# Kernel tuning notes

Hardware: AMD Instinct MI355X
Metric: run time of the kernel (lower is better)

The kernel has to match this reference:

```python
import jax, jax.numpy as jnp
import numpy as np

B, T, DM, H, DH = 4, 2048, 1024, 16, 64
DI = H * DH
CLIP = 1.0
LN_EPS = 1e-5


def setup_inputs() -> dict:
    key = jax.random.key(0)
    ks = jax.random.split(key, 9)

    def xav(k, shape):  # xavier_uniform, fan_in=shape[1], fan_out=shape[0]
        lim = float(np.sqrt(6.0 / (shape[0] + shape[1])))
        return jax.random.uniform(k, shape, jnp.float32, -lim, lim)

    def kai(k, shape):  # default nn.Linear weight init
        lim = float(1.0 / np.sqrt(shape[1]))
        return jax.random.uniform(k, shape, jnp.float32, -lim, lim)

    return {
        "x": jax.random.normal(ks[0], (B, T, DM), jnp.float32),
        "Wq": xav(ks[1], (DI, DM)),
        "Wk": xav(ks[2], (DI, DM)),
        "Wv": xav(ks[3], (DI, DM)),
        "Wa": kai(ks[4], (DI, DM)), "ba": jnp.full((DI,), 3.0, jnp.float32),
        "Wb": kai(ks[5], (H, DM)), "bb": jnp.zeros((H,), jnp.float32),
        "Wg": kai(ks[6], (H, DM)), "bg": jnp.zeros((H,), jnp.float32),
        "WaR": kai(ks[7], (DI, DM)), "baR": jnp.full((DI,), 3.0, jnp.float32),
        "Wo": xav(ks[8], (DM, DI)),
        "ln_w": jnp.ones((DM,), jnp.float32),
        "ln_b": jnp.zeros((DM,), jnp.float32),
    }


def reference(x, Wq, Wk, Wv, Wa, ba, Wb, bb, Wg, bg, WaR, baR, Wo, ln_w, ln_b):
    Bs, Ts, _ = x.shape
    residual = x
    # LayerNorm
    mu = jnp.mean(x, -1, keepdims=True)
    var = jnp.mean((x - mu) ** 2, -1, keepdims=True)
    xn = (x - mu) / jnp.sqrt(var + LN_EPS) * ln_w + ln_b

    q = (xn @ Wq.T).reshape(Bs, Ts, H, DH)
    k = (xn @ Wk.T).reshape(Bs, Ts, H, DH)
    v = (xn @ Wv.T).reshape(Bs, Ts, H, DH)
    alpha = jax.nn.sigmoid(xn @ Wa.T + ba).reshape(Bs, Ts, H, DH)
    aR = jax.nn.sigmoid(xn @ WaR.T + baR).reshape(Bs, Ts, H, DH)
    beta = jax.nn.sigmoid(xn @ Wb.T + bb)   # (B,T,H)
    gamma = jax.nn.sigmoid(xn @ Wg.T + bg)  # (B,T,H)

    tm = lambda a: jnp.moveaxis(a, 1, 0)  # time-major for scan
    xs = (tm(q), tm(k), tm(v), tm(alpha), tm(aR), tm(beta), tm(gamma))
    S0 = jnp.zeros((Bs, H, DH, DH), x.dtype)

    def step(carry, inp):
        S, R = carry
        q_t, k_t, v_t, a_t, aR_t, b_t, g_t = inp  # (B,H,d) / (B,H)
        kn = k_t / jnp.maximum(jnp.linalg.norm(k_t, axis=-1, keepdims=True), 1e-12)
        # residual target from previous state: r = clip(v - S^T k)
        pred = jnp.einsum('bhji,bhj->bhi', S, kn)
        r = jnp.clip(v_t - pred, -CLIP, CLIP)
        # primary state: S = diag(alpha) S; S += beta k (v - k^T S)
        S = a_t[..., None] * S
        kp = jnp.einsum('bhd,bhde->bhe', kn, S)
        S = S + b_t[..., None, None] * kn[..., None] * (v_t - kp)[..., None, :]
        o = jnp.einsum('bhji,bhj->bhi', S, q_t)
        # residual state
        R = aR_t[..., None] * R
        kpR = jnp.einsum('bhd,bhde->bhe', kn, R)
        R = R + g_t[..., None, None] * kn[..., None] * (r - kpR)[..., None, :]
        o = o + jnp.einsum('bhji,bhj->bhi', R, q_t)
        return (S, R), o

    _, os = jax.lax.scan(step, (S0, S0), xs)  # os: (T,B,H,d)
    out = jnp.moveaxis(os, 0, 1).reshape(Bs, Ts, DI) @ Wo.T
    return out + residual  # dropout is identity at inference
```

## Files before the change

kernel.cpp:

```cpp
#include <hip/hip_runtime.h>
#include <hip/hip_fp16.h>

#define B_SZ 4
#define T_SEQ 2048
#define NH 16
#define HD 64
#define DMODEL 1024
#define MTOT (B_SZ * T_SEQ)

typedef __bf16 bf16x8 __attribute__((ext_vector_type(8)));
typedef float f32x4 __attribute__((ext_vector_type(4)));
typedef float f32x2 __attribute__((ext_vector_type(2)));
typedef _Float16 f16x4 __attribute__((ext_vector_type(4)));

__device__ __forceinline__ unsigned short f2bf(float f) {
    union { float f; unsigned int i; } c; c.f = f;
    unsigned int u = c.i;
    u += 0x7fffu + ((u >> 16) & 1u);
    return (unsigned short)(u >> 16);
}
__device__ __forceinline__ float sigm(float x) { return 1.f / (1.f + __expf(-x)); }

__device__ __forceinline__ void dma16(const void* g, void* l) {
    __builtin_amdgcn_global_load_lds(
        (const __attribute__((address_space(1))) void*)g,
        (__attribute__((address_space(3))) void*)l, 16, 0, 0);
}

template <int CTRL>
__device__ __forceinline__ float dppadd(float x) {
    int v = __builtin_amdgcn_update_dpp(0, __builtin_bit_cast(int, x), CTRL, 0xf, 0xf, false);
    return x + __builtin_bit_cast(float, v);
}
__device__ __forceinline__ float rowsum16(float x) {
    x = dppadd<0x128>(x);
    x = dppadd<0x124>(x);
    x = dppadd<0x122>(x);
    x = dppadd<0x121>(x);
    return x;
}

__device__ __forceinline__ void rowsum3(float& a, float& b, float& c) {
    asm volatile(
        "s_nop 1\n\t"
        "v_add_f32_dpp %0, %0, %0 row_ror:8 row_mask:0xf bank_mask:0xf\n\t"
        "v_add_f32_dpp %1, %1, %1 row_ror:8 row_mask:0xf bank_mask:0xf\n\t"
        "v_add_f32_dpp %2, %2, %2 row_ror:8 row_mask:0xf bank_mask:0xf\n\t"
        "v_add_f32_dpp %0, %0, %0 row_ror:4 row_mask:0xf bank_mask:0xf\n\t"
        "v_add_f32_dpp %1, %1, %1 row_ror:4 row_mask:0xf bank_mask:0xf\n\t"
        "v_add_f32_dpp %2, %2, %2 row_ror:4 row_mask:0xf bank_mask:0xf\n\t"
        "v_add_f32_dpp %0, %0, %0 row_ror:2 row_mask:0xf bank_mask:0xf\n\t"
        "v_add_f32_dpp %1, %1, %1 row_ror:2 row_mask:0xf bank_mask:0xf\n\t"
        "v_add_f32_dpp %2, %2, %2 row_ror:2 row_mask:0xf bank_mask:0xf\n\t"
        "v_add_f32_dpp %0, %0, %0 row_ror:1 row_mask:0xf bank_mask:0xf\n\t"
        "v_add_f32_dpp %1, %1, %1 row_ror:1 row_mask:0xf bank_mask:0xf\n\t"
        "v_add_f32_dpp %2, %2, %2 row_ror:1 row_mask:0xf bank_mask:0xf"
        : "+v"(a), "+v"(b), "+v"(c));
}

__global__ __launch_bounds__(256, 1) void k_ln(const float* __restrict__ x,
                                               const float* __restrict__ lnw,
                                               const float* __restrict__ lnb,
                                               unsigned short* __restrict__ xn) {
    const int m = blockIdx.x;
    const int t = threadIdx.x;
    float4 xv = ((const float4*)(x + (size_t)m * DMODEL))[t];
    float s = xv.x + xv.y + xv.z + xv.w;
    float s2 = xv.x * xv.x + xv.y * xv.y + xv.z * xv.z + xv.w * xv.w;
#pragma unroll
    for (int off = 32; off >= 1; off >>= 1) {
        s += __shfl_xor(s, off);
        s2 += __shfl_xor(s2, off);
    }
    __shared__ float red[8];
    const int wid = t >> 6;
    if ((t & 63) == 0) { red[wid] = s; red[4 + wid] = s2; }
    __syncthreads();
    if (t == 0) {
        float su = red[0] + red[1] + red[2] + red[3];
        float sq = red[4] + red[5] + red[6] + red[7];
        float mu = su * (1.f / DMODEL);
        float var = sq * (1.f / DMODEL) - mu * mu;
        red[0] = mu;
        red[1] = rsqrtf(var + 1e-5f);
    }
    __syncthreads();
    float mu = red[0], rstd = red[1];
    float4 w4 = ((const float4*)lnw)[t];
    float4 b4 = ((const float4*)lnb)[t];
    ushort4 o;
    o.x = f2bf((xv.x - mu) * rstd * w4.x + b4.x);
    o.y = f2bf((xv.y - mu) * rstd * w4.y + b4.y);
    o.z = f2bf((xv.z - mu) * rstd * w4.z + b4.z);
    o.w = f2bf((xv.w - mu) * rstd * w4.w + b4.w);
    ((ushort4*)(xn + (size_t)m * DMODEL))[t] = o;
}

struct WPtrs { const float* p0; const float* p1; const float* p2; const float* p3; const float* p4; };

__global__ __launch_bounds__(256, 1) void k_wconv(WPtrs w, unsigned short* __restrict__ dst) {
    const int plane = blockIdx.y;
    const float* src = plane == 0 ? w.p0 : plane == 1 ? w.p1 : plane == 2 ? w.p2
                                                             : plane == 3 ? w.p3 : w.p4;
    const size_t i = ((size_t)blockIdx.x * 256 + threadIdx.x) * 8;
    float4 f0 = *(const float4*)(src + i);
    float4 f1 = *(const float4*)(src + i + 4);
    uint4 o;
    o.x = (unsigned)f2bf(f0.x) | ((unsigned)f2bf(f0.y) << 16);
    o.y = (unsigned)f2bf(f0.z) | ((unsigned)f2bf(f0.w) << 16);
    o.z = (unsigned)f2bf(f1.x) | ((unsigned)f2bf(f1.y) << 16);
    o.w = (unsigned)f2bf(f1.z) | ((unsigned)f2bf(f1.w) << 16);
    *(uint4*)(dst + (size_t)plane * 1048576 + i) = o;
}

__global__ __launch_bounds__(256, 1) void k_cvt1(const float* __restrict__ src,
                                                 unsigned short* __restrict__ dst) {
    const size_t i = ((size_t)blockIdx.x * 256 + threadIdx.x) * 8;
    float4 f0 = *(const float4*)(src + i);
    float4 f1 = *(const float4*)(src + i + 4);
    uint4 o;
    o.x = (unsigned)f2bf(f0.x) | ((unsigned)f2bf(f0.y) << 16);
    o.y = (unsigned)f2bf(f0.z) | ((unsigned)f2bf(f0.w) << 16);
    o.z = (unsigned)f2bf(f1.x) | ((unsigned)f2bf(f1.y) << 16);
    o.w = (unsigned)f2bf(f1.z) | ((unsigned)f2bf(f1.w) << 16);
    *(uint4*)(dst + i) = o;
}

template <int KDIM>
__device__ __forceinline__ void gemm128(const unsigned short* __restrict__ A,
                                        const unsigned short* __restrict__ Bw,
                                        int m0, int n0, f32x4 acc[4][4]) {
    __shared__ __align__(16) unsigned short sA[128 * 32];
    __shared__ __align__(16) unsigned short sB[128 * 32];

    const int t = threadIdx.x;
    const int lane = t & 63;
    const int wv = t >> 6;
    const int wm = wv >> 1, wn = wv & 1;
    const int ml = lane & 15, kq = lane >> 4;

#pragma unroll
    for (int i = 0; i < 4; i++)
#pragma unroll
        for (int j = 0; j < 4; j++) {
            f32x4 z; z[0] = 0.f; z[1] = 0.f; z[2] = 0.f; z[3] = 0.f;
            acc[i][j] = z;
        }

    const unsigned short* pA = A + (size_t)m0 * KDIM;
    const unsigned short* pB = Bw + (size_t)n0 * KDIM;
    const unsigned short* gA0 = pA + (size_t)(t >> 2) * KDIM + (t & 3) * 8;
    const unsigned short* gA1 = gA0 + (size_t)64 * KDIM;
    const unsigned short* gB0 = pB + (size_t)(t >> 2) * KDIM + (t & 3) * 8;
    const unsigned short* gB1 = gB0 + (size_t)64 * KDIM;
    unsigned short* lA0 = sA + wv * 512;
    unsigned short* lA1 = lA0 + 2048;
    unsigned short* lB0 = sB + wv * 512;
    unsigned short* lB1 = lB0 + 2048;

    for (int kb = 0; kb < KDIM / 32; kb++) {
        const int ko = kb * 32;
        dma16(gA0 + ko, lA0);
        dma16(gA1 + ko, lA1);
        dma16(gB0 + ko, lB0);
        dma16(gB1 + ko, lB1);
        __syncthreads();
        bf16x8 af[4], bfr[4];
#pragma unroll
        for (int mt = 0; mt < 4; mt++)
            af[mt] = *(const bf16x8*)&sA[(wm * 64 + mt * 16 + ml) * 32 + kq * 8];
#pragma unroll
        for (int nt = 0; nt < 4; nt++)
            bfr[nt] = *(const bf16x8*)&sB[(wn * 64 + nt * 16 + ml) * 32 + kq * 8];
#pragma unroll
        for (int mt = 0; mt < 4; mt++)
#pragma unroll
            for (int nt = 0; nt < 4; nt++)
                acc[mt][nt] = __builtin_amdgcn_mfma_f32_16x16x32_bf16(af[mt], bfr[nt], acc[mt][nt], 0, 0, 0);
        __syncthreads();
    }
}

template <typename OT>
__global__ __launch_bounds__(256, 1) void k_proj(const unsigned short* __restrict__ xn,
                                                 const unsigned short* __restrict__ wbf,
                                                 const float* __restrict__ ba,
                                                 const float* __restrict__ baR,
                                                 OT* __restrict__ qo, OT* __restrict__ ko,
                                                 OT* __restrict__ vo, OT* __restrict__ ao,
                                                 OT* __restrict__ aRo) {
    const int m0 = blockIdx.x * 128;
    const int yt = blockIdx.y;
    const int widx = yt >> 3;
    const int n0 = (yt & 7) * 128;
    const unsigned short* W = wbf + (size_t)widx * 1048576;
    f32x4 acc[4][4];
    gemm128<1024>(xn, W, m0, n0, acc);

    OT* outp = widx == 0 ? qo : widx == 1 ? ko : widx == 2 ? vo : widx == 3 ? ao : aRo;
    const float* bias = (widx == 3) ? ba : (widx == 4) ? baR : (const float*)0;
    const int lane = threadIdx.x & 63;
    const int wv = threadIdx.x >> 6;
    const int wm = wv >> 1, wn = wv & 1;
    const int ml = lane & 15, kq = lane >> 4;
#pragma unroll
    for (int mt = 0; mt < 4; mt++)
#pragma unroll
        for (int nt = 0; nt < 4; nt++) {
            const int rowg = m0 + wm * 64 + mt * 16 + kq * 4;
            const int colg = n0 + wn * 64 + nt * 16 + ml;
            float bval = bias ? bias[colg] : 0.f;
#pragma unroll
            for (int r = 0; r < 4; r++) {
                float v = acc[mt][nt][r];
                if (widx >= 3) v = sigm(v + bval);
                outp[(size_t)(rowg + r) * DMODEL + colg] = (OT)v;
            }
        }
}

__global__ __launch_bounds__(256, 1) void k_bg(const unsigned short* __restrict__ xn,
                                               const float* __restrict__ Wb,
                                               const float* __restrict__ bb,
                                               const float* __restrict__ Wg,
                                               const float* __restrict__ bgp,
                                               f32x2* __restrict__ bgpk) {
    const int m = blockIdx.x;
    const int t = threadIdx.x;
    const int h = t >> 4, seg = t & 15;
    const ushort4* xr = (const ushort4*)(xn + (size_t)m * DMODEL + seg * 64);
    const float4* wbr = (const float4*)(Wb + (size_t)h * DMODEL + seg * 64);
    const float4* wgr = (const float4*)(Wg + (size_t)h * DMODEL + seg * 64);
    float db = 0.f, dg = 0.f;
#pragma unroll
    for (int u = 0; u < 16; u++) {
        ushort4 a = xr[u];
        float4 w1 = wbr[u], w2 = wgr[u];
        union { unsigned int i; float f; } c0, c1, c2, c3;
        c0.i = ((unsigned int)a.x) << 16; c1.i = ((unsigned int)a.y) << 16;
        c2.i = ((unsigned int)a.z) << 16; c3.i = ((unsigned int)a.w) << 16;
        db += c0.f * w1.x + c1.f * w1.y + c2.f * w1.z + c3.f * w1.w;
        dg += c0.f * w2.x + c1.f * w2.y + c2.f * w2.z + c3.f * w2.w;
    }
#pragma unroll
    for (int off = 1; off < 16; off <<= 1) {
        db += __shfl_xor(db, off);
        dg += __shfl_xor(dg, off);
    }
    if (seg == 0) {
        f32x2 o;
        o[0] = sigm(db + bb[h]);
        o[1] = sigm(dg + bgp[h]);
        bgpk[(size_t)m * NH + h] = o;
    }
}

__global__ __launch_bounds__(256, 1) void k_prep16(__half* __restrict__ kb) {
    const int row = blockIdx.x * 16 + (threadIdx.x >> 4);
    const int tr = threadIdx.x & 15;
    const int bh = row >> 11, t = row & 2047;
    const size_t idx = ((size_t)((bh >> 4) * T_SEQ + t)) * DMODEL + (bh & 15) * 64 + tr * 4;
    f16x4 k4 = *(const f16x4*)((const __half*)kb + idx);
    float k0 = (float)k4[0], k1 = (float)k4[1], k2 = (float)k4[2], k3 = (float)k4[3];
    float ss = k0 * k0 + k1 * k1 + k2 * k2 + k3 * k3;
    ss = rowsum16(ss);
    float inv = 1.f / fmaxf(sqrtf(ss), 1e-12f);
    f16x4 o;
    o[0] = (_Float16)(k0 * inv); o[1] = (_Float16)(k1 * inv);
    o[2] = (_Float16)(k2 * inv); o[3] = (_Float16)(k3 * inv);
    *(f16x4*)(kb + idx) = o;
}

__global__ __launch_bounds__(256, 1) void k_prep32(float* __restrict__ kb) {
    const int row = blockIdx.x * 16 + (threadIdx.x >> 4);
    const int tr = threadIdx.x & 15;
    const int bh = row >> 11, t = row & 2047;
    const size_t idx = ((size_t)((bh >> 4) * T_SEQ + t)) * DMODEL + (bh & 15) * 64 + tr * 4;
    f32x4 k4 = *(const f32x4*)(kb + idx);
    float ss = k4[0] * k4[0] + k4[1] * k4[1] + k4[2] * k4[2] + k4[3] * k4[3];
    ss = rowsum16(ss);
    float inv = 1.f / fmaxf(sqrtf(ss), 1e-12f);
    f32x4 o;
    o[0] = k4[0] * inv; o[1] = k4[1] * inv; o[2] = k4[2] * inv; o[3] = k4[3] * inv;
    *(f32x4*)(kb + idx) = o;
}

__global__ __launch_bounds__(256, 1) void k_scan32(const float* __restrict__ qb,
                                                   const float* __restrict__ knb,
                                                   const float* __restrict__ vb,
                                                   const float* __restrict__ ab,
                                                   const float* __restrict__ aRb,
                                                   const f32x2* __restrict__ bgpk,
                                                   unsigned short* __restrict__ ob) {
    const int blk = blockIdx.x;
    const int bh = blk & 63, cg = blk >> 6;
    const int b = bh >> 4, h = bh & 15;
    const int t = threadIdx.x;
    const int col = t >> 4, tr = t & 15;
    const int ii = cg * 16 + col;
    const int j0 = tr * 4;

    const size_t blkoff = (size_t)b * T_SEQ * DMODEL + h * 64;
    const float* pq = qb + blkoff;
    const float* pk = knb + blkoff;
    const float* pa = ab + blkoff;
    const float* pr = aRb + blkoff;
    const float* pvb = vb + blkoff;
    const f32x2* pbg = bgpk + (size_t)b * T_SEQ * NH + h;
    unsigned short* obp = ob + blkoff + ii;

    f32x2 S01 = {0.f, 0.f}, S23 = {0.f, 0.f}, R01 = {0.f, 0.f}, R23 = {0.f, 0.f};

    f32x4 rk[6], rq[6], ra[6], rr[6];
    float rv[6];
    f32x2 rbg[6];

#pragma unroll
    for (int p = 0; p < 6; p++) {
        const size_t vo = (size_t)p * DMODEL;
        rk[p] = *(const f32x4*)(pk + vo + j0);
        rq[p] = *(const f32x4*)(pq + vo + j0);
        ra[p] = *(const f32x4*)(pa + vo + j0);
        rr[p] = *(const f32x4*)(pr + vo + j0);
        rv[p] = pvb[vo + ii];
        rbg[p] = pbg[(size_t)p * NH];
    }

    float oA, oB, oC;

#define SCAN_BODY32(P, ODEST)                                                       \
    {                                                                               \
        const f32x2 kn01 = {rk[P][0], rk[P][1]}, kn23 = {rk[P][2], rk[P][3]};       \
        const f32x2 a01 = {ra[P][0], ra[P][1]}, a23 = {ra[P][2], ra[P][3]};         \
        const f32x2 x01 = {rr[P][0], rr[P][1]}, x23 = {rr[P][2], rr[P][3]};         \
        const f32x2 q01 = {rq[P][0], rq[P][1]}, q23 = {rq[P][2], rq[P][3]};         \
        const float vc = rv[P];                                                     \
        const float beta = rbg[P][0], gamma = rbg[P][1];                            \
        const f32x2 Sd01 = a01 * S01, Sd23 = a23 * S23;                             \
        const f32x2 Rd01 = x01 * R01, Rd23 = x23 * R23;                             \
        const f32x2 pv2 = S01 * kn01 + S23 * kn23;                                  \
        const f32x2 kp2 = Sd01 * kn01 + Sd23 * kn23;                                \
        const f32x2 kR2 = Rd01 * kn01 + Rd23 * kn23;                                \
        float pred = pv2[0] + pv2[1];                                               \
        float kp = kp2[0] + kp2[1];                                                 \
        float kpR = kR2[0] + kR2[1];                                                \
        rowsum3(pred, kp, kpR);                                                     \
        const float rres = fminf(fmaxf(vc - pred, -1.f), 1.f);                      \
        const float cS = beta * (vc - kp);                                          \
        const float cR = gamma * (rres - kpR);                                      \
        const f32x2 cS2 = {cS, cS}, cR2 = {cR, cR};                                 \
        S01 = cS2 * kn01 + Sd01; S23 = cS2 * kn23 + Sd23;                           \
        R01 = cR2 * kn01 + Rd01; R23 = cR2 * kn23 + Rd23;                           \
        const f32x2 ov = (S01 + R01) * q01 + (S23 + R23) * q23;                     \
        ODEST = ov[0] + ov[1];                                                      \
              \
        {                                                                           \
            const int sp = (st + (P) + 6) & (T_SEQ - 1);                            \
            const size_t vo = (size_t)sp * DMODEL;                                  \
            rk[P] = *(const f32x4*)(pk + vo + j0);                                  \
            rq[P] = *(const f32x4*)(pq + vo + j0);                                  \
            ra[P] = *(const f32x4*)(pa + vo + j0);                                  \
            rr[P] = *(const f32x4*)(pr + vo + j0);                                  \
            rv[P] = pvb[vo + ii];                                                   \
            rbg[P] = pbg[(size_t)sp * NH];                                          \
        }                                                                           \
    }

#define FLUSH3(SBASE)                                                               \
    {                                                                               \
        rowsum3(oA, oB, oC);                                                        \
        if (tr == 0) {                                                              \
            if ((SBASE) < T_SEQ)     obp[(size_t)(SBASE) * DMODEL] = f2bf(oA);      \
            if ((SBASE) + 1 < T_SEQ) obp[(size_t)((SBASE) + 1) * DMODEL] = f2bf(oB);\
            if ((SBASE) + 2 < T_SEQ) obp[(size_t)((SBASE) + 2) * DMODEL] = f2bf(oC);\
        }                                                                           \
    }

    for (int st = 0; st < T_SEQ; st += 6) {
        SCAN_BODY32(0, oA)
        SCAN_BODY32(1, oB)
        SCAN_BODY32(2, oC)
        FLUSH3(st)
        SCAN_BODY32(3, oA)
        SCAN_BODY32(4, oB)
        SCAN_BODY32(5, oC)
        FLUSH3(st + 3)
    }
#undef SCAN_BODY32
#undef FLUSH3
}

__global__ __launch_bounds__(256, 1) void k_scan16(const __half* __restrict__ qb,
                                                   const __half* __restrict__ knb,
                                                   const __half* __restrict__ vb,
                                                   const __half* __restrict__ ab,
                                                   const __half* __restrict__ aRb,
                                                   const f32x2* __restrict__ bgpk,
                                                   unsigned short* __restrict__ ob) {
    const int blk = blockIdx.x;
    const int bh = blk & 63, cg = blk >> 6;
    const int b = bh >> 4, h = bh & 15;
    const int t = threadIdx.x;
    const int col = t >> 4, tr = t & 15;
    const int ii = cg * 16 + col;
    const int j0 = tr * 4;

    const size_t vecbase = ((size_t)b * T_SEQ) * DMODEL + h * 64 + j0;
    const size_t vbase = ((size_t)b * T_SEQ) * DMODEL + h * 64 + ii;
    const size_t bgbase = ((size_t)b * T_SEQ) * NH + h;

    const __half* pk = knb + vecbase;
    const __half* pq = qb + vecbase;
    const __half* pa = ab + vecbase;
    const __half* pr = aRb + vecbase;

    float S0 = 0, S1 = 0, S2 = 0, S3 = 0, R0 = 0, R1 = 0, R2 = 0, R3 = 0;

    f16x4 rk[6], rq[6], ra[6], rr[6];
    __half rv[6];
    f32x2 rbg[6];
    f32x4 fkn[6], fq[6], fa[6], fr[6];
    float fv[6];

#pragma unroll
    for (int p = 0; p < 6; p++) {
        const size_t voff = (size_t)p * DMODEL;
        rk[p] = *(const f16x4*)(pk + voff);
        rq[p] = *(const f16x4*)(pq + voff);
        ra[p] = *(const f16x4*)(pa + voff);
        rr[p] = *(const f16x4*)(pr + voff);
        rv[p] = vb[vbase + voff];
        rbg[p] = bgpk[bgbase + (size_t)p * NH];
    }
    fkn[0][0] = (float)rk[0][0]; fkn[0][1] = (float)rk[0][1]; fkn[0][2] = (float)rk[0][2]; fkn[0][3] = (float)rk[0][3];
    fq[0][0] = (float)rq[0][0]; fq[0][1] = (float)rq[0][1]; fq[0][2] = (float)rq[0][2]; fq[0][3] = (float)rq[0][3];
    fa[0][0] = (float)ra[0][0]; fa[0][1] = (float)ra[0][1]; fa[0][2] = (float)ra[0][2]; fa[0][3] = (float)ra[0][3];
    fr[0][0] = (float)rr[0][0]; fr[0][1] = (float)rr[0][1]; fr[0][2] = (float)rr[0][2]; fr[0][3] = (float)rr[0][3];
    fv[0] = (float)rv[0];

#define SCAN_BODY(P, PN)                                                              \
    {                                                                                 \
        const int s = st + (P);                                                       \
        const float beta = rbg[P][0], gamma = rbg[P][1];                              \
        {                                                                             \
            const size_t voff = (size_t)((s + 6) & (T_SEQ - 1)) * DMODEL;             \
            rk[P] = *(const f16x4*)(pk + voff);                                       \
            rq[P] = *(const f16x4*)(pq + voff);                                       \
            ra[P] = *(const f16x4*)(pa + voff);                                       \
            rr[P] = *(const f16x4*)(pr + voff);                                       \
            rv[P] = vb[vbase + voff];                                                 \
        }                                                                             \
        fkn[PN][0] = (float)rk[PN][0]; fkn[PN][1] = (float)rk[PN][1];                 \
        fkn[PN][2] = (float)rk[PN][2]; fkn[PN][3] = (float)rk[PN][3];                 \
        fq[PN][0] = (float)rq[PN][0]; fq[PN][1] = (float)rq[PN][1];                   \
        fq[PN][2] = (float)rq[PN][2]; fq[PN][3] = (float)rq[PN][3];                   \
        fa[PN][0] = (float)ra[PN][0]; fa[PN][1] = (float)ra[PN][1];                   \
        fa[PN][2] = (float)ra[PN][2]; fa[PN][3] = (float)ra[PN][3];                   \
        fr[PN][0] = (float)rr[PN][0]; fr[PN][1] = (float)rr[PN][1];                   \
        fr[PN][2] = (float)rr[PN][2]; fr[PN][3] = (float)rr[PN][3];                   \
        fv[PN] = (float)rv[PN];                                                       \
        {                                                                             \
            const float kn0 = fkn[P][0], kn1 = fkn[P][1], kn2 = fkn[P][2], kn3 = fkn[P][3]; \
            const float a0 = fa[P][0], a1 = fa[P][1], a2 = fa[P][2], a3 = fa[P][3];   \
            const float x0 = fr[P][0], x1 = fr[P][1], x2 = fr[P][2], x3 = fr[P][3];   \
            const float vc = fv[P];                                                   \
            float pred = S0 * kn0 + S1 * kn1 + S2 * kn2 + S3 * kn3;                   \
            float Sd0 = a0 * S0, Sd1 = a1 * S1, Sd2 = a2 * S2, Sd3 = a3 * S3;         \
            float Rd0 = x0 * R0, Rd1 = x1 * R1, Rd2 = x2 * R2, Rd3 = x3 * R3;         \
            float kp = Sd0 * kn0 + Sd1 * kn1 + Sd2 * kn2 + Sd3 * kn3;                 \
            float kpR = Rd0 * kn0 + Rd1 * kn1 + Rd2 * kn2 + Rd3 * kn3;                \
            pred = rowsum16(pred);                                                    \
            kp = rowsum16(kp);                                                        \
            kpR = rowsum16(kpR);                                                      \
            const float rres = fminf(fmaxf(vc - pred, -1.f), 1.f);                    \
            const float cS = beta * (vc - kp);                                        \
            const float cR = gamma * (rres - kpR);                                    \
            S0 = fmaf(cS, kn0, Sd0); S1 = fmaf(cS, kn1, Sd1);                         \
            S2 = fmaf(cS, kn2, Sd2); S3 = fmaf(cS, kn3, Sd3);                         \
            R0 = fmaf(cR, kn0, Rd0); R1 = fmaf(cR, kn1, Rd1);                         \
            R2 = fmaf(cR, kn2, Rd2); R3 = fmaf(cR, kn3, Rd3);                         \
            float o = (S0 + R0) * fq[P][0] + (S1 + R1) * fq[P][1] +                   \
                      (S2 + R2) * fq[P][2] + (S3 + R3) * fq[P][3];                    \
            o = rowsum16(o);                                                          \
            if (tr == 0 && s < T_SEQ)                                                 \
                ob[vbase + (size_t)s * DMODEL] = f2bf(o);                             \
        }                                                                             \
        rbg[P] = bgpk[bgbase + (size_t)((s + 6) & (T_SEQ - 1)) * NH];                 \
    }

    for (int st = 0; st < T_SEQ; st += 6) {
        SCAN_BODY(0, 1)
        SCAN_BODY(1, 2)
        SCAN_BODY(2, 3)
        SCAN_BODY(3, 4)
        SCAN_BODY(4, 5)
        SCAN_BODY(5, 0)
    }
#undef SCAN_BODY
}

__global__ __launch_bounds__(256, 1) void k_out(const unsigned short* __restrict__ ob,
                                                const unsigned short* __restrict__ wobf,
                                                const float* __restrict__ x,
                                                float* __restrict__ out) {
    const int m0 = blockIdx.x * 128;
    const int n0 = blockIdx.y * 128;
    f32x4 acc[4][4];
    gemm128<1024>(ob, wobf, m0, n0, acc);
    const int lane = threadIdx.x & 63;
    const int wv = threadIdx.x >> 6;
    const int wm = wv >> 1, wn = wv & 1;
    const int ml = lane & 15, kq = lane >> 4;
#pragma unroll
    for (int mt = 0; mt < 4; mt++)
#pragma unroll
        for (int nt = 0; nt < 4; nt++) {
            const int rowg = m0 + wm * 64 + mt * 16 + kq * 4;
            const int colg = n0 + wn * 64 + nt * 16 + ml;
#pragma unroll
            for (int r = 0; r < 4; r++) {
                size_t idx = (size_t)(rowg + r) * DMODEL + colg;
                out[idx] = acc[mt][nt][r] + x[idx];
            }
        }
}

extern "C" void kernel_launch(void* const* d_in, const int* in_sizes, int n_in,
                              void* d_out, int out_size, void* d_ws, size_t ws_size,
                              hipStream_t stream) {
    const float* x = (const float*)d_in[0];
    const float* Wq = (const float*)d_in[1];
    const float* Wk = (const float*)d_in[2];
    const float* Wv = (const float*)d_in[3];
    const float* Wa = (const float*)d_in[4];
    const float* ba = (const float*)d_in[5];
    const float* Wb = (const float*)d_in[6];
    const float* bb = (const float*)d_in[7];
    const float* Wg = (const float*)d_in[8];
    const float* bg = (const float*)d_in[9];
    const float* WaR = (const float*)d_in[10];
    const float* baR = (const float*)d_in[11];
    const float* Wo = (const float*)d_in[12];
    const float* lnw = (const float*)d_in[13];
    const float* lnb = (const float*)d_in[14];

    const size_t SZH = 16777216ULL;
    const size_t SZF = 33554432ULL;
    const size_t need32 = 5 * SZF + SZH + 2097152ULL;
    const size_t need16 = 6 * SZH + 2097152ULL;

    char* ws = (char*)d_ws;
    unsigned short* wbf = (unsigned short*)d_out;
    WPtrs wp{Wq, Wk, Wv, Wa, WaR};

    if (ws_size >= need32) {
        float* qb = (float*)(ws + 0 * SZF);
        float* kb = (float*)(ws + 1 * SZF);
        float* vb = (float*)(ws + 2 * SZF);
        float* ab = (float*)(ws + 3 * SZF);
        float* aRb = (float*)(ws + 4 * SZF);
        unsigned short* xn = (unsigned short*)(ws + 5 * SZF);
        f32x2* bgpk = (f32x2*)(ws + 5 * SZF + SZH);
        unsigned short* wobf = (unsigned short*)qb;

        k_wconv<<<dim3(512, 5), dim3(256), 0, stream>>>(wp, wbf);
        k_ln<<<dim3(MTOT), dim3(256), 0, stream>>>(x, lnw, lnb, xn);
        k_proj<float><<<dim3(64, 40), dim3(256), 0, stream>>>(xn, wbf, ba, baR, qb, kb, vb, ab, aRb);
        k_bg<<<dim3(MTOT), dim3(256), 0, stream>>>(xn, Wb, bb, Wg, bg, bgpk);
        k_prep32<<<dim3(MTOT * NH / 16), dim3(256), 0, stream>>>(kb);
        k_scan32<<<dim3(256), dim3(256), 0, stream>>>(qb, kb, vb, ab, aRb, bgpk, xn);
        k_cvt1<<<dim3(512), dim3(256), 0, stream>>>(Wo, wobf);
        k_out<<<dim3(64, 8), dim3(256), 0, stream>>>(xn, wobf, x, (float*)d_out);
    } else if (ws_size >= need16) {
        __half* qb = (__half*)(ws + 0 * SZH);
        __half* kb = (__half*)(ws + 1 * SZH);
        __half* vb = (__half*)(ws + 2 * SZH);
        __half* ab = (__half*)(ws + 3 * SZH);
        __half* aRb = (__half*)(ws + 4 * SZH);
        unsigned short* xn = (unsigned short*)(ws + 5 * SZH);
        f32x2* bgpk = (f32x2*)(ws + 6 * SZH);
        unsigned short* wobf = (unsigned short*)qb;

        k_wconv<<<dim3(512, 5), dim3(256), 0, stream>>>(wp, wbf);
        k_ln<<<dim3(MTOT), dim3(256), 0, stream>>>(x, lnw, lnb, xn);
        k_proj<_Float16><<<dim3(64, 40), dim3(256), 0, stream>>>(
            xn, wbf, ba, baR, (_Float16*)qb, (_Float16*)kb, (_Float16*)vb, (_Float16*)ab, (_Float16*)aRb);
        k_bg<<<dim3(MTOT), dim3(256), 0, stream>>>(xn, Wb, bb, Wg, bg, bgpk);
        k_prep16<<<dim3(MTOT * NH / 16), dim3(256), 0, stream>>>(kb);
        k_scan16<<<dim3(256), dim3(256), 0, stream>>>(qb, kb, vb, ab, aRb, bgpk, xn);
        k_cvt1<<<dim3(512), dim3(256), 0, stream>>>(Wo, wobf);
        k_out<<<dim3(64, 8), dim3(256), 0, stream>>>(xn, wobf, x, (float*)d_out);
    }
}
```

Before: 831.3 us.

## Double-buffer LDS tiles in gemm128 to overlap global loads with MFMA

Result: no change. 826.1 us (-0.6%).

```diff
diff --git a/kernel.cpp b/kernel.cpp
--- a/kernel.cpp
+++ b/kernel.cpp
@@ -130,8 +130,8 @@
 __device__ __forceinline__ void gemm128(const unsigned short* __restrict__ A,
                                         const unsigned short* __restrict__ Bw,
                                         int m0, int n0, f32x4 acc[4][4]) {
-    __shared__ __align__(16) unsigned short sA[128 * 32];
-    __shared__ __align__(16) unsigned short sB[128 * 32];
+    __shared__ __align__(16) unsigned short sA[2 * 128 * 32];
+    __shared__ __align__(16) unsigned short sB[2 * 128 * 32];
 
     const int t = threadIdx.x;
     const int lane = t & 63;
@@ -158,26 +158,43 @@
     unsigned short* lB0 = sB + wv * 512;
     unsigned short* lB1 = lB0 + 2048;
 
-    for (int kb = 0; kb < KDIM / 32; kb++) {
-        const int ko = kb * 32;
-        dma16(gA0 + ko, lA0);
-        dma16(gA1 + ko, lA1);
-        dma16(gB0 + ko, lB0);
-        dma16(gB1 + ko, lB1);
-        __syncthreads();
+    constexpr int NK = KDIM / 32;
+
+    dma16(gA0, lA0);
+    dma16(gA1, lA1);
+    dma16(gB0, lB0);
+    dma16(gB1, lB1);
+    asm volatile("s_waitcnt vmcnt(0)" ::: "memory");
+    __builtin_amdgcn_s_barrier();
+
+    int cur = 0;
+    for (int kb = 0; kb < NK; kb++) {
+        const int nxt = cur ^ 1;
+        if (kb + 1 < NK) {
+            const int ko = (kb + 1) * 32;
+            const int bo = nxt * 4096;
+            dma16(gA0 + ko, lA0 + bo);
+            dma16(gA1 + ko, lA1 + bo);
+            dma16(gB0 + ko, lB0 + bo);
+            dma16(gB1 + ko, lB1 + bo);
+        }
+        const unsigned short* bA = sA + cur * 4096;
+        const unsigned short* bB = sB + cur * 4096;
         bf16x8 af[4], bfr[4];
 #pragma unroll
         for (int mt = 0; mt < 4; mt++)
-            af[mt] = *(const bf16x8*)&sA[(wm * 64 + mt * 16 + ml) * 32 + kq * 8];
+            af[mt] = *(const bf16x8*)&bA[(wm * 64 + mt * 16 + ml) * 32 + kq * 8];
 #pragma unroll
         for (int nt = 0; nt < 4; nt++)
-            bfr[nt] = *(const bf16x8*)&sB[(wn * 64 + nt * 16 + ml) * 32 + kq * 8];
+            bfr[nt] = *(const bf16x8*)&bB[(wn * 64 + nt * 16 + ml) * 32 + kq * 8];
 #pragma unroll
         for (int mt = 0; mt < 4; mt++)
 #pragma unroll
             for (int nt = 0; nt < 4; nt++)
                 acc[mt][nt] = __builtin_amdgcn_mfma_f32_16x16x32_bf16(af[mt], bfr[nt], acc[mt][nt], 0, 0, 0);
-        __syncthreads();
+        asm volatile("s_waitcnt vmcnt(0) lgkmcnt(0)" ::: "memory");
+        __builtin_amdgcn_s_barrier();
+        cur = nxt;
     }
 }
 
```
